# Performance work log

Hardware: AMD Instinct MI355X
Metric: run time of the kernel (lower is better)

The kernel has to match this reference:

```python
import jax, jax.numpy as jnp
import numpy as np
from jax import lax

D_STATE = 16
D_CONV = 4
EXPAND = 2


def setup_inputs() -> dict:
    key = jax.random.key(0)
    ks = jax.random.split(key, 12)
    B, C, H, W = 8, 192, 32, 32
    d_inner = EXPAND * C            # 384
    dt_rank = (C + 15) // 16        # 12
    s = lambda k, shape, sc=0.02: jax.random.normal(k, shape, jnp.float32) * sc
    return {
        "x": jax.random.normal(ks[0], (B, C, H, W), jnp.float32),
        # proj_in: 1x1 Conv2d (in_ch -> out_ch)
        "proj_w": s(ks[1], (C, C)),
        "proj_b": s(ks[2], (C,)),
        # Mamba params (mamba_ssm defaults, biases per reference impl)
        "in_proj_w": s(ks[3], (2 * d_inner, C)),
        "conv_w": s(ks[4], (d_inner, D_CONV)),
        "conv_b": s(ks[5], (d_inner,)),
        "xproj_w": s(ks[6], (dt_rank + 2 * D_STATE, d_inner)),
        "dtproj_w": s(ks[7], (d_inner, dt_rank), 0.1),
        "dtproj_b": s(ks[8], (d_inner,), 0.5),
        "A_log": jnp.log(jnp.tile(jnp.arange(1, D_STATE + 1, dtype=jnp.float32), (d_inner, 1))),
        "Dp": jnp.ones((d_inner,), jnp.float32),
        "out_w": s(ks[9], (C, d_inner)),
    }


def _forward(x, proj_w, proj_b, in_proj_w, conv_w, conv_b, xproj_w,
             dtproj_w, dtproj_b, A_log, Dp, out_w):
    B, C, H, W = x.shape
    L = H * W
    # proj_in (1x1 conv) + flatten 'b c h w -> b (h w) c'
    u = jnp.einsum('bchw,oc->bhwo', x, proj_w).reshape(B, L, -1) + proj_b
    # Mamba layer
    xz = u @ in_proj_w.T                      # [B,L,2*d_inner]
    xin, z = jnp.split(xz, 2, axis=-1)
    # causal depthwise conv1d (kernel D_CONV), truncated to L
    xp = jnp.pad(xin, ((0, 0), (D_CONV - 1, 0), (0, 0)))
    xc = conv_b + sum(conv_w[:, k] * xp[:, k:k + L, :] for k in range(D_CONV))
    xc = jax.nn.silu(xc)
    # input-dependent dt, B, C
    dt_rank = dtproj_w.shape[1]
    x_dbl = xc @ xproj_w.T                    # [B,L,dt_rank+2*n]
    dtr, Bt, Ct = jnp.split(x_dbl, [dt_rank, dt_rank + D_STATE], axis=-1)
    dt = jax.nn.softplus(dtr @ dtproj_w.T + dtproj_b)   # [B,L,d_inner]
    A = -jnp.exp(A_log)                       # [d_inner, n]
    deltaA = jnp.exp(dt[..., None] * A)                          # [B,L,d,n]
    dBx = dt[..., None] * Bt[:, :, None, :] * xc[..., None]      # [B,L,d,n]

    def step(h, ins):
        dA, dbx, ct = ins                      # [B,d,n],[B,d,n],[B,n]
        h = dA * h + dbx
        return h, jnp.einsum('bdn,bn->bd', h, ct)

    h0 = jnp.zeros((B, A.shape[0], D_STATE), xc.dtype)
    _, ys = lax.scan(step, h0, (deltaA.transpose(1, 0, 2, 3),
                                dBx.transpose(1, 0, 2, 3),
                                Ct.transpose(1, 0, 2)))
    y = ys.transpose(1, 0, 2) + xc * Dp        # [B,L,d_inner]
    y = y * jax.nn.silu(z)
    out = y @ out_w.T                          # [B,L,C]
    # 'b (h w) c -> b c h w'
    return out.reshape(B, H, W, C).transpose(0, 3, 1, 2)


def reference(x, proj_w, proj_b, in_proj_w, conv_w, conv_b, xproj_w,
              dtproj_w, dtproj_b, A_log, Dp, out_w):
    return _forward(x, proj_w, proj_b, in_proj_w, conv_w, conv_b, xproj_w,
                    dtproj_w, dtproj_b, A_log, Dp, out_w)
```

## Files before the change

kernel.cpp:

```cpp
#include <hip/hip_runtime.h>
#include <math.h>

#define BB 8
#define CC 192
#define LL 1024
#define RT 8192
#define DI 384
#define DT_RANK 12
#define NS 16
#define NSEG 16
#define SEGL 64

typedef __attribute__((ext_vector_type(8))) short bf16x8;
typedef __attribute__((ext_vector_type(4))) float f32x4;

__device__ __forceinline__ unsigned short f2bf(float f) {
    unsigned u = __float_as_uint(f);
    unsigned r = (u + 0x7FFFu + ((u >> 16) & 1u)) >> 16;
    return (unsigned short)r;
}
__device__ __forceinline__ float bf2f(unsigned short h) {
    return __uint_as_float(((unsigned)h) << 16);
}

__device__ __forceinline__ void gload_lds16(const float* g, float* l) {
    __builtin_amdgcn_global_load_lds(
        (const __attribute__((address_space(1))) void*)(g),
        (__attribute__((address_space(3))) void*)(l),
        16, 0, 0);
}

__device__ __forceinline__ float row_sum16(float v) {
    v += __int_as_float(__builtin_amdgcn_update_dpp(0, __float_as_int(v), 0x140, 0xF, 0xF, true));
    v += __int_as_float(__builtin_amdgcn_update_dpp(0, __float_as_int(v), 0x141, 0xF, 0xF, true));
    v += __int_as_float(__builtin_amdgcn_update_dpp(0, __float_as_int(v), 0x4E,  0xF, 0xF, true));
    v += __int_as_float(__builtin_amdgcn_update_dpp(0, __float_as_int(v), 0xB1,  0xF, 0xF, true));
    return v;
}

__global__ void fuse_w_kernel(const float* __restrict__ in_proj_w,
                              const float* __restrict__ proj_w,
                              const float* __restrict__ proj_b,
                              unsigned short* __restrict__ W2hi,
                              unsigned short* __restrict__ W2lo,
                              float* __restrict__ bias2,
                              float* __restrict__ xdT) {
    int j = blockIdx.x;
    int cp = threadIdx.x;
    int gtid = j * CC + cp;
    for (int i = gtid; i < 44 * RT; i += 768 * CC) xdT[i] = 0.f;
    __shared__ float wrow[CC];
    wrow[cp] = in_proj_w[j * CC + cp];
    __syncthreads();
    float acc = 0.f;
#pragma unroll 4
    for (int c = 0; c < CC; ++c) acc = fmaf(wrow[c], proj_w[c * CC + cp], acc);
    unsigned short h = f2bf(acc);
    W2hi[j * CC + cp] = h;
    W2lo[j * CC + cp] = f2bf(acc - bf2f(h));
    if (cp == 0) {
        float b = 0.f;
        for (int c = 0; c < CC; ++c) b = fmaf(wrow[c], proj_b[c], b);
        bias2[j] = b;
    }
}

__global__ __launch_bounds__(256) void gemm_xz(const float* __restrict__ x,
                                               const unsigned short* __restrict__ W2hi,
                                               const unsigned short* __restrict__ W2lo,
                                               const float* __restrict__ bias2,
                                               float* __restrict__ xzT) {
    __shared__ unsigned short xhi[2048];
    __shared__ unsigned short xlo[2048];
    int r0 = blockIdx.x * 64;
    int j0 = blockIdx.y * 64;
    int b  = r0 >> 10;
    int l0 = r0 & 1023;
    int tid = threadIdx.x;
    int lane = tid & 63;
    int wid = tid >> 6;
    int jw = j0 + wid * 16;
    const float* xb = x + b * CC * LL + l0 + lane;
    f32x4 z4 = {0.f, 0.f, 0.f, 0.f};
    f32x4 acc[4] = {z4, z4, z4, z4};
    int arow = jw + (lane & 15);
    int akb  = (lane >> 4) * 8;
    for (int ks = 0; ks < 6; ++ks) {
        int k0 = ks * 32;
        float v[8];
#pragma unroll
        for (int e = 0; e < 8; ++e) v[e] = xb[(k0 + wid * 8 + e) * LL];
        union U8 { unsigned short u[8]; bf16x8 v8; } hv, lv;
#pragma unroll
        for (int e = 0; e < 8; ++e) {
            unsigned short h = f2bf(v[e]);
            hv.u[e] = h;
            lv.u[e] = f2bf(v[e] - bf2f(h));
        }
        *(bf16x8*)&xhi[(wid * 64 + lane) * 8] = hv.v8;
        *(bf16x8*)&xlo[(wid * 64 + lane) * 8] = lv.v8;
        __syncthreads();
        int aoff = arow * CC + k0 + akb;
        bf16x8 ah = *(const bf16x8*)&W2hi[aoff];
        bf16x8 al = *(const bf16x8*)&W2lo[aoff];
#pragma unroll
        for (int rt = 0; rt < 4; ++rt) {
            int boff = ((lane >> 4) * 64 + rt * 16 + (lane & 15)) * 8;
            bf16x8 bh = *(const bf16x8*)&xhi[boff];
            bf16x8 bl = *(const bf16x8*)&xlo[boff];
            acc[rt] = __builtin_amdgcn_mfma_f32_16x16x32_bf16(ah, bh, acc[rt], 0, 0, 0);
            acc[rt] = __builtin_amdgcn_mfma_f32_16x16x32_bf16(ah, bl, acc[rt], 0, 0, 0);
            acc[rt] = __builtin_amdgcn_mfma_f32_16x16x32_bf16(al, bh, acc[rt], 0, 0, 0);
        }
        __syncthreads();
    }
    bool is_z = (j0 >= DI);
#pragma unroll
    for (int rt = 0; rt < 4; ++rt) {
        int rbase = r0 + rt * 16 + (lane & 15);
#pragma unroll
        for (int reg = 0; reg < 4; ++reg) {
            int j = jw + (lane >> 4) * 4 + reg;
            float o = acc[rt][reg] + bias2[j];
            if (is_z) o = __fdividef(o, 1.f + __expf(-o));
            xzT[j * RT + rbase] = o;
        }
    }
}

__global__ __launch_bounds__(512) void xproj_conv_gemm(const float* __restrict__ xzT,
                                                       const float* __restrict__ conv_w,
                                                       const float* __restrict__ conv_b,
                                                       const float* __restrict__ aw,
                                                       float* __restrict__ xcT,
                                                       float* __restrict__ xdT) {
    __shared__ float Bs[32][64];
    int col0 = blockIdx.x * 64;
    int kbase = blockIdx.y * 192;
    int tid = threadIdx.x;
    int col = tid & 63, mg = tid >> 6;
    int mb = mg * 6;
    const float* ar[6];
#pragma unroll
    for (int m = 0; m < 6; ++m) ar[m] = aw + min(mb + m, 43) * DI + kbase;
    float acc[6] = {};
    int ks = tid >> 4, c4 = (tid & 15) * 4;
    bool atL0 = ((col0 & 1023) == 0) && (c4 == 0);
    for (int k0 = 0; k0 < 192; k0 += 32) {
        int dch = kbase + k0 + ks;
        const float* src = xzT + (size_t)dch * RT + col0 + c4;
        float4 cur = *(const float4*)src;
        float4 prev = make_float4(0.f, 0.f, 0.f, 0.f);
        if (!atL0) prev = *(const float4*)(src - 4);
        float4 w4 = *(const float4*)&conv_w[dch * 4];
        float bb = conv_b[dch];
        float v0 = bb + w4.w * cur.x + w4.z * prev.w + w4.y * prev.z + w4.x * prev.y;
        float v1 = bb + w4.w * cur.y + w4.z * cur.x  + w4.y * prev.w + w4.x * prev.z;
        float v2 = bb + w4.w * cur.z + w4.z * cur.y  + w4.y * cur.x  + w4.x * prev.w;
        float v3 = bb + w4.w * cur.w + w4.z * cur.z  + w4.y * cur.y  + w4.x * cur.x;
        float4 o;
        o.x = __fdividef(v0, 1.f + __expf(-v0));
        o.y = __fdividef(v1, 1.f + __expf(-v1));
        o.z = __fdividef(v2, 1.f + __expf(-v2));
        o.w = __fdividef(v3, 1.f + __expf(-v3));
        *(float4*)&Bs[ks][c4] = o;
        *(float4*)&xcT[(size_t)dch * RT + col0 + c4] = o;
        __syncthreads();
#pragma unroll
        for (int k = 0; k < 32; ++k) {
            float bv = Bs[k][col];
#pragma unroll
            for (int m = 0; m < 6; ++m)
                acc[m] = fmaf(ar[m][k0 + k], bv, acc[m]);
        }
        __syncthreads();
    }
#pragma unroll
    for (int m = 0; m < 6; ++m)
        if (mb + m < 44)
            atomicAdd(&xdT[(mb + m) * RT + col0 + col], acc[m]);
}

__global__ __launch_bounds__(256) void scan_part1(const float* __restrict__ xdT,
                                                  const float* __restrict__ xcT,
                                                  const float* __restrict__ dtw,
                                                  const float* __restrict__ dtb,
                                                  const float* __restrict__ A_log,
                                                  float* __restrict__ P,
                                                  float* __restrict__ Hf) {
    __shared__ float dt_s[16][20], g_s[16][20], B_s[16][20];
    __shared__ float dtr_s[12][17];
    __shared__ float dtw_s[192];
    __shared__ float dtb_s[16];
    int seg = blockIdx.x, d0 = blockIdx.y * 16, b = blockIdx.z;
    int row0 = b * LL + seg * SEGL;
    int tid = threadIdx.x;
    int lane = tid & 63;
    int n = lane & 15;
    int dl = ((tid >> 6) << 2) | (lane >> 4);
    int tdd = tid >> 4, ti = tid & 15;
    if (tid < 192) dtw_s[tid] = dtw[d0 * DT_RANK + tid];
    if (tid < 16)  dtb_s[tid] = dtb[d0 + tid];
    float a = -__expf(A_log[(d0 + dl) * NS + n]);
    float h = 0.f, sdt = 0.f;
    for (int ch = 0; ch < 4; ++ch) {
        int r = row0 + ch * 16;
        float xv = xcT[(d0 + tdd) * RT + r + ti];
        B_s[tdd][ti] = xdT[(12 + tdd) * RT + r + ti];
        if (tid < 192) dtr_s[tid >> 4][ti] = xdT[(tid >> 4) * RT + r + ti];
        __syncthreads();
        float acc = dtb_s[tdd];
#pragma unroll
        for (int rr = 0; rr < DT_RANK; ++rr)
            acc = fmaf(dtr_s[rr][ti], dtw_s[tdd * DT_RANK + rr], acc);
        float dtv = fmaxf(acc, 0.f) + __logf(1.f + __expf(-fabsf(acc)));
        dt_s[tdd][ti] = dtv;
        g_s[tdd][ti]  = dtv * xv;
        __syncthreads();
        float dv[16], gb[16];
#pragma unroll
        for (int q = 0; q < 4; ++q) {
            float4 d4 = *(const float4*)&dt_s[dl][q * 4];
            float4 g4 = *(const float4*)&g_s[dl][q * 4];
            float4 b4 = *(const float4*)&B_s[n][q * 4];
            dv[q * 4 + 0] = d4.x; dv[q * 4 + 1] = d4.y;
            dv[q * 4 + 2] = d4.z; dv[q * 4 + 3] = d4.w;
            gb[q * 4 + 0] = g4.x * b4.x; gb[q * 4 + 1] = g4.y * b4.y;
            gb[q * 4 + 2] = g4.z * b4.z; gb[q * 4 + 3] = g4.w * b4.w;
        }
        __syncthreads();
        float eh[16];
#pragma unroll
        for (int i = 0; i < 16; ++i) eh[i] = __expf(dv[i] * a);
#pragma unroll
        for (int i = 0; i < 16; ++i) {
            sdt += dv[i];
            h = fmaf(eh[i], h, gb[i]);
        }
    }
    int idx = ((seg * BB + b) * DI + d0 + dl) * NS + n;
    P[idx] = __expf(a * sdt);
    Hf[idx] = h;
}

__global__ __launch_bounds__(256) void scan_part2(const float* __restrict__ xdT,
                                                  const float* __restrict__ xcT,
                                                  const float* __restrict__ zsT,
                                                  const float* __restrict__ dtw,
                                                  const float* __restrict__ dtb,
                                                  const float* __restrict__ P,
                                                  const float* __restrict__ Hf,
                                                  const float* __restrict__ A_log,
                                                  const float* __restrict__ Dp,
                                                  float* __restrict__ yT) {
    __shared__ float dt_s[16][20], g_s[16][20], B_s[16][20], C_s[16][20];
    __shared__ float dtr_s[12][17];
    __shared__ float dtw_s[192];
    __shared__ float dtb_s[16];
    int seg = blockIdx.x, d0 = blockIdx.y * 16, b = blockIdx.z;
    int row0 = b * LL + seg * SEGL;
    int tid = threadIdx.x;
    int lane = tid & 63;
    int n = lane & 15;
    int dl = ((tid >> 6) << 2) | (lane >> 4);
    int d = d0 + dl;
    int tdd = tid >> 4, ti = tid & 15;
    if (tid < 192) dtw_s[tid] = dtw[d0 * DT_RANK + tid];
    if (tid < 16)  dtb_s[tid] = dtb[d0 + tid];
    float a = -__expf(A_log[d * NS + n]);
    float Dpd = Dp[d];
    float h = 0.f;
    for (int s = 0; s < seg; ++s) {
        int off = ((s * BB + b) * DI + d) * NS + n;
        h = fmaf(P[off], h, Hf[off]);
    }
    for (int ch = 0; ch < 4; ++ch) {
        int r = row0 + ch * 16;
        float xr = xcT[(size_t)d * RT + r + n];
        float zr = zsT[(size_t)d * RT + r + n];
        float xv = xcT[(d0 + tdd) * RT + r + ti];
        B_s[tdd][ti] = xdT[(12 + tdd) * RT + r + ti];
        C_s[tdd][ti] = xdT[(28 + tdd) * RT + r + ti];
        if (tid < 192) dtr_s[tid >> 4][ti] = xdT[(tid >> 4) * RT + r + ti];
        __syncthreads();
        float acc = dtb_s[tdd];
#pragma unroll
        for (int rr = 0; rr < DT_RANK; ++rr)
            acc = fmaf(dtr_s[rr][ti], dtw_s[tdd * DT_RANK + rr], acc);
        float dtv = fmaxf(acc, 0.f) + __logf(1.f + __expf(-fabsf(acc)));
        dt_s[tdd][ti] = dtv;
        g_s[tdd][ti]  = dtv * xv;
        __syncthreads();
        float dv[16], gb[16], cv[16];
#pragma unroll
        for (int q = 0; q < 4; ++q) {
            float4 d4 = *(const float4*)&dt_s[dl][q * 4];
            float4 g4 = *(const float4*)&g_s[dl][q * 4];
            float4 b4 = *(const float4*)&B_s[n][q * 4];
            float4 c4 = *(const float4*)&C_s[n][q * 4];
            dv[q * 4 + 0] = d4.x; dv[q * 4 + 1] = d4.y;
            dv[q * 4 + 2] = d4.z; dv[q * 4 + 3] = d4.w;
            gb[q * 4 + 0] = g4.x * b4.x; gb[q * 4 + 1] = g4.y * b4.y;
            gb[q * 4 + 2] = g4.z * b4.z; gb[q * 4 + 3] = g4.w * b4.w;
            cv[q * 4 + 0] = c4.x; cv[q * 4 + 1] = c4.y;
            cv[q * 4 + 2] = c4.z; cv[q * 4 + 3] = c4.w;
        }
        __syncthreads();
        float eh[16];
#pragma unroll
        for (int i = 0; i < 16; ++i) eh[i] = __expf(dv[i] * a);
        float yacc = 0.f;
#pragma unroll
        for (int i = 0; i < 16; ++i) {
            h = fmaf(eh[i], h, gb[i]);
            float v = row_sum16(h * cv[i]);
            yacc = (n == i) ? v : yacc;
        }
        yT[(size_t)d * RT + r + n] = fmaf(xr, Dpd, yacc) * zr;
    }
}

__global__ __launch_bounds__(256) void gemm_out(const float* __restrict__ yT,
                                                const float* __restrict__ out_w,
                                                float* __restrict__ out) {
    __shared__ float As[16][64];
    __shared__ float Bs[16][68];
    int r0 = blockIdx.x * 64;
    int c0 = blockIdx.y * 64;
    int b = r0 >> 10, l0 = r0 & 1023;
    int tid = threadIdx.x;
    int tx = tid & 15;
    int ty = tid >> 4;
    float acc[4][4] = {};
    for (int k0 = 0; k0 < DI; k0 += 16) {
        {
            gload_lds16(&yT[(k0 + (tid >> 4)) * RT + r0 + (tid & 15) * 4],
                        ((float*)As) + tid * 4);
        }
        {
            int c = tid >> 2, kc = (tid & 3) * 4;
            float4 v = *(const float4*)&out_w[(c0 + c) * DI + k0 + kc];
            Bs[kc + 0][c] = v.x; Bs[kc + 1][c] = v.y;
            Bs[kc + 2][c] = v.z; Bs[kc + 3][c] = v.w;
        }
        __syncthreads();
#pragma unroll
        for (int k = 0; k < 16; ++k) {
            float4 av = *(const float4*)&As[k][tx * 4];
            float4 bv = *(const float4*)&Bs[k][ty * 4];
            acc[0][0] = fmaf(bv.x, av.x, acc[0][0]);
            acc[0][1] = fmaf(bv.x, av.y, acc[0][1]);
            acc[0][2] = fmaf(bv.x, av.z, acc[0][2]);
            acc[0][3] = fmaf(bv.x, av.w, acc[0][3]);
            acc[1][0] = fmaf(bv.y, av.x, acc[1][0]);
            acc[1][1] = fmaf(bv.y, av.y, acc[1][1]);
            acc[1][2] = fmaf(bv.y, av.z, acc[1][2]);
            acc[1][3] = fmaf(bv.y, av.w, acc[1][3]);
            acc[2][0] = fmaf(bv.z, av.x, acc[2][0]);
            acc[2][1] = fmaf(bv.z, av.y, acc[2][1]);
            acc[2][2] = fmaf(bv.z, av.z, acc[2][2]);
            acc[2][3] = fmaf(bv.z, av.w, acc[2][3]);
            acc[3][0] = fmaf(bv.w, av.x, acc[3][0]);
            acc[3][1] = fmaf(bv.w, av.y, acc[3][1]);
            acc[3][2] = fmaf(bv.w, av.z, acc[3][2]);
            acc[3][3] = fmaf(bv.w, av.w, acc[3][3]);
        }
        __syncthreads();
    }
    float* ob = out + b * CC * LL;
#pragma unroll
    for (int ic = 0; ic < 4; ++ic) {
        float4 o;
        o.x = acc[ic][0]; o.y = acc[ic][1]; o.z = acc[ic][2]; o.w = acc[ic][3];
        *(float4*)&ob[(c0 + ty * 4 + ic) * LL + l0 + tx * 4] = o;
    }
}

extern "C" void kernel_launch(void* const* d_in, const int* in_sizes, int n_in,
                              void* d_out, int out_size, void* d_ws, size_t ws_size,
                              hipStream_t stream) {
    const float* x         = (const float*)d_in[0];
    const float* proj_w    = (const float*)d_in[1];
    const float* proj_b    = (const float*)d_in[2];
    const float* in_proj_w = (const float*)d_in[3];
    const float* conv_w    = (const float*)d_in[4];
    const float* conv_b    = (const float*)d_in[5];
    const float* xproj_w   = (const float*)d_in[6];
    const float* dtproj_w  = (const float*)d_in[7];
    const float* dtproj_b  = (const float*)d_in[8];
    const float* A_log     = (const float*)d_in[9];
    const float* Dp        = (const float*)d_in[10];
    const float* out_w     = (const float*)d_in[11];
    float* out = (float*)d_out;

    float* ws    = (float*)d_ws;
    unsigned short* W2hi = (unsigned short*)ws;
    unsigned short* W2lo = (unsigned short*)(ws + 73728);
    float* bias2 = ws + 147456;
    float* xzT   = bias2 + 768;
    float* xcT   = xzT + 6291456;
    float* yT    = xcT + 3145728;
    float* xdT   = yT + 3145728;
    float* P     = xdT + 360448;
    float* Hf    = P + 786432;
    float* zsT   = xzT + DI * RT;

    fuse_w_kernel<<<768, 192, 0, stream>>>(in_proj_w, proj_w, proj_b,
                                           W2hi, W2lo, bias2, xdT);
    gemm_xz<<<dim3(128, 12), 256, 0, stream>>>(x, W2hi, W2lo, bias2, xzT);
    xproj_conv_gemm<<<dim3(128, 2), 512, 0, stream>>>(xzT, conv_w, conv_b,
                                                      xproj_w, xcT, xdT);
    scan_part1<<<dim3(16, 24, 8), 256, 0, stream>>>(xdT, xcT, dtproj_w, dtproj_b,
                                                    A_log, P, Hf);
    scan_part2<<<dim3(16, 24, 8), 256, 0, stream>>>(xdT, xcT, zsT, dtproj_w, dtproj_b,
                                                    P, Hf, A_log, Dp, yT);
    gemm_out<<<dim3(128, 3), 256, 0, stream>>>(yT, out_w, out);
}
```

Baseline: 210.0 us.

## Use split-bf16 MFMA for output projection GEMM

Moves the final output GEMM from an FP32 FMA tile loop onto bf16 MFMA instructions. The out_w weights are split into hi/lo bf16 pairs in the weight-prep kernel, and y is split the same way on the fly. Three MFMAs per tile (hi*hi, hi*lo, lo*hi) keep accuracy close to fp32. The cost is that y is now converted per block in the kernel, and the output stores become scalar strided writes instead of float4.

```diff
diff --git a/kernel.cpp b/kernel.cpp
--- a/kernel.cpp
+++ b/kernel.cpp
@@ -23,13 +23,6 @@
     return __uint_as_float(((unsigned)h) << 16);
 }
 
-__device__ __forceinline__ void gload_lds16(const float* g, float* l) {
-    __builtin_amdgcn_global_load_lds(
-        (const __attribute__((address_space(1))) void*)(g),
-        (__attribute__((address_space(3))) void*)(l),
-        16, 0, 0);
-}
-
 __device__ __forceinline__ float row_sum16(float v) {
     v += __int_as_float(__builtin_amdgcn_update_dpp(0, __float_as_int(v), 0x140, 0xF, 0xF, true));
     v += __int_as_float(__builtin_amdgcn_update_dpp(0, __float_as_int(v), 0x141, 0xF, 0xF, true));
@@ -41,14 +34,23 @@
 __global__ void fuse_w_kernel(const float* __restrict__ in_proj_w,
                               const float* __restrict__ proj_w,
                               const float* __restrict__ proj_b,
+                              const float* __restrict__ out_w,
                               unsigned short* __restrict__ W2hi,
                               unsigned short* __restrict__ W2lo,
+                              unsigned short* __restrict__ owhi,
+                              unsigned short* __restrict__ owlo,
                               float* __restrict__ bias2,
                               float* __restrict__ xdT) {
     int j = blockIdx.x;
     int cp = threadIdx.x;
     int gtid = j * CC + cp;
     for (int i = gtid; i < 44 * RT; i += 768 * CC) xdT[i] = 0.f;
+    if (j < DI) {
+        float v = out_w[cp * DI + j];
+        unsigned short h = f2bf(v);
+        owhi[cp * DI + j] = h;
+        owlo[cp * DI + j] = f2bf(v - bf2f(h));
+    }
     __shared__ float wrow[CC];
     wrow[cp] = in_proj_w[j * CC + cp];
     __syncthreads();
@@ -321,58 +323,62 @@
 }
 
 __global__ __launch_bounds__(256) void gemm_out(const float* __restrict__ yT,
-                                                const float* __restrict__ out_w,
+                                                const unsigned short* __restrict__ owhi,
+                                                const unsigned short* __restrict__ owlo,
                                                 float* __restrict__ out) {
-    __shared__ float As[16][64];
-    __shared__ float Bs[16][68];
+    __shared__ unsigned short yhi[2048];
+    __shared__ unsigned short ylo[2048];
     int r0 = blockIdx.x * 64;
     int c0 = blockIdx.y * 64;
-    int b = r0 >> 10, l0 = r0 & 1023;
+    int b  = r0 >> 10;
+    int l0 = r0 & 1023;
     int tid = threadIdx.x;
-    int tx = tid & 15;
-    int ty = tid >> 4;
-    float acc[4][4] = {};
-    for (int k0 = 0; k0 < DI; k0 += 16) {
-        {
-            gload_lds16(&yT[(k0 + (tid >> 4)) * RT + r0 + (tid & 15) * 4],
-                        ((float*)As) + tid * 4);
-        }
-        {
-            int c = tid >> 2, kc = (tid & 3) * 4;
-            float4 v = *(const float4*)&out_w[(c0 + c) * DI + k0 + kc];
-            Bs[kc + 0][c] = v.x; Bs[kc + 1][c] = v.y;
-            Bs[kc + 2][c] = v.z; Bs[kc + 3][c] = v.w;
-        }
-        __syncthreads();
-#pragma unroll
-        for (int k = 0; k < 16; ++k) {
-            float4 av = *(const float4*)&As[k][tx * 4];
-            float4 bv = *(const float4*)&Bs[k][ty * 4];
-            acc[0][0] = fmaf(bv.x, av.x, acc[0][0]);
-            acc[0][1] = fmaf(bv.x, av.y, acc[0][1]);
-            acc[0][2] = fmaf(bv.x, av.z, acc[0][2]);
-            acc[0][3] = fmaf(bv.x, av.w, acc[0][3]);
-            acc[1][0] = fmaf(bv.y, av.x, acc[1][0]);
-            acc[1][1] = fmaf(bv.y, av.y, acc[1][1]);
-            acc[1][2] = fmaf(bv.y, av.z, acc[1][2]);
-            acc[1][3] = fmaf(bv.y, av.w, acc[1][3]);
-            acc[2][0] = fmaf(bv.z, av.x, acc[2][0]);
-            acc[2][1] = fmaf(bv.z, av.y, acc[2][1]);
-            acc[2][2] = fmaf(bv.z, av.z, acc[2][2]);
-            acc[2][3] = fmaf(bv.z, av.w, acc[2][3]);
-            acc[3][0] = fmaf(bv.w, av.x, acc[3][0]);
-            acc[3][1] = fmaf(bv.w, av.y, acc[3][1]);
-            acc[3][2] = fmaf(bv.w, av.z, acc[3][2]);
-            acc[3][3] = fmaf(bv.w, av.w, acc[3][3]);
+    int lane = tid & 63;
+    int wid = tid >> 6;
+    int cw = c0 + wid * 16;
+    const float* yb = yT + r0 + lane;
+    f32x4 z4 = {0.f, 0.f, 0.f, 0.f};
+    f32x4 acc[4] = {z4, z4, z4, z4};
+    int arow = cw + (lane & 15);
+    int akb  = (lane >> 4) * 8;
+    for (int ks = 0; ks < 12; ++ks) {
+        int k0 = ks * 32;
+        float v[8];
+#pragma unroll
+        for (int e = 0; e < 8; ++e) v[e] = yb[(size_t)(k0 + wid * 8 + e) * RT];
+        union U8 { unsigned short u[8]; bf16x8 v8; } hv, lv;
+#pragma unroll
+        for (int e = 0; e < 8; ++e) {
+            unsigned short h = f2bf(v[e]);
+            hv.u[e] = h;
+            lv.u[e] = f2bf(v[e] - bf2f(h));
+        }
+        *(bf16x8*)&yhi[(wid * 64 + lane) * 8] = hv.v8;
+        *(bf16x8*)&ylo[(wid * 64 + lane) * 8] = lv.v8;
+        __syncthreads();
+        int aoff = arow * DI + k0 + akb;
+        bf16x8 ah = *(const bf16x8*)&owhi[aoff];
+        bf16x8 al = *(const bf16x8*)&owlo[aoff];
+#pragma unroll
+        for (int rt = 0; rt < 4; ++rt) {
+            int boff = ((lane >> 4) * 64 + rt * 16 + (lane & 15)) * 8;
+            bf16x8 bh = *(const bf16x8*)&yhi[boff];
+            bf16x8 bl = *(const bf16x8*)&ylo[boff];
+            acc[rt] = __builtin_amdgcn_mfma_f32_16x16x32_bf16(ah, bh, acc[rt], 0, 0, 0);
+            acc[rt] = __builtin_amdgcn_mfma_f32_16x16x32_bf16(ah, bl, acc[rt], 0, 0, 0);
+            acc[rt] = __builtin_amdgcn_mfma_f32_16x16x32_bf16(al, bh, acc[rt], 0, 0, 0);
         }
         __syncthreads();
     }
     float* ob = out + b * CC * LL;
 #pragma unroll
-    for (int ic = 0; ic < 4; ++ic) {
-        float4 o;
-        o.x = acc[ic][0]; o.y = acc[ic][1]; o.z = acc[ic][2]; o.w = acc[ic][3];
-        *(float4*)&ob[(c0 + ty * 4 + ic) * LL + l0 + tx * 4] = o;
+    for (int rt = 0; rt < 4; ++rt) {
+        int lbase = l0 + rt * 16 + (lane & 15);
+#pragma unroll
+        for (int reg = 0; reg < 4; ++reg) {
+            int c = cw + (lane >> 4) * 4 + reg;
+            ob[c * LL + lbase] = acc[rt][reg];
+        }
     }
 }
 
@@ -403,10 +409,12 @@
     float* xdT   = yT + 3145728;
     float* P     = xdT + 360448;
     float* Hf    = P + 786432;
+    unsigned short* owhi = (unsigned short*)(Hf + 786432);
+    unsigned short* owlo = (unsigned short*)(Hf + 786432 + 36864);
     float* zsT   = xzT + DI * RT;
 
-    fuse_w_kernel<<<768, 192, 0, stream>>>(in_proj_w, proj_w, proj_b,
-                                           W2hi, W2lo, bias2, xdT);
+    fuse_w_kernel<<<768, 192, 0, stream>>>(in_proj_w, proj_w, proj_b, out_w,
+                                           W2hi, W2lo, owhi, owlo, bias2, xdT);
     gemm_xz<<<dim3(128, 12), 256, 0, stream>>>(x, W2hi, W2lo, bias2, xzT);
     xproj_conv_gemm<<<dim3(128, 2), 512, 0, stream>>>(xzT, conv_w, conv_b,
                                                       xproj_w, xcT, xdT);
@@ -414,5 +422,5 @@
                                                     A_log, P, Hf);
     scan_part2<<<dim3(16, 24, 8), 256, 0, stream>>>(xdT, xcT, zsT, dtproj_w, dtproj_b,
                                                     P, Hf, A_log, Dp, yT);
-    gemm_out<<<dim3(128, 3), 256, 0, stream>>>(yT, out_w, out);
-}
+    gemm_out<<<dim3(128, 3), 256, 0, stream>>>(yT, owhi, owlo, out);
+}
```

Result: faster. 202.2 us (-3.7%).
